# Kernel optimization log

Measured on AMD Instinct MI355X. Metric: run time of the kernel, lower is better.

## Reference

```python
import jax, jax.numpy as jnp
import numpy as np
from jax import lax

NUM_CLASSES = 20
NUM_ANCHORS = 5
COORDS = 4
NMS_TH = 0.45
PRE_TH = 0.005
FEAT_STRIDE = 32.0
BIASES = jnp.array([[1.08, 1.19], [3.42, 4.41], [6.63, 11.38],
                    [9.42, 5.11], [16.62, 10.52]], dtype=jnp.float32)  # [A,2]


def setup_inputs() -> dict:
    key = jax.random.key(0)
    B, H, W = 16, 26, 26
    C = (NUM_CLASSES + COORDS + 1) * NUM_ANCHORS  # 125
    x = jax.random.normal(key, (B, C, H, W), dtype=jnp.float32)
    im_info = jnp.array([480.0, 640.0], dtype=jnp.float32)  # (orig_h, orig_w)
    return {"x": x, "im_info": im_info}


def _pairwise_iou(b):
    # b: [N,4] center-format (cx, cy, w, h)
    x1 = b[:, 0] - b[:, 2] * 0.5
    y1 = b[:, 1] - b[:, 3] * 0.5
    x2 = b[:, 0] + b[:, 2] * 0.5
    y2 = b[:, 1] + b[:, 3] * 0.5
    area = (x2 - x1) * (y2 - y1)
    iw = jnp.maximum(jnp.minimum(x2[:, None], x2[None, :]) - jnp.maximum(x1[:, None], x1[None, :]), 0.0)
    ih = jnp.maximum(jnp.minimum(y2[:, None], y2[None, :]) - jnp.maximum(y1[:, None], y1[None, :]), 0.0)
    inter = iw * ih
    return inter / (area[:, None] + area[None, :] - inter + 1e-12)


def _nms_scores(boxes, scores):
    # greedy single-class NMS; returns scores with pre-threshold + suppressed boxes zeroed
    N = scores.shape[0]
    s = jnp.where(scores < PRE_TH, 0.0, scores)
    order = jnp.argsort(-s)
    ss = s[order]
    iou = lax.stop_gradient(_pairwise_iou(boxes[order]))  # [N,N]
    idx = jnp.arange(N)

    def body(i, keep):
        ki = keep[i] & (ss[i] > 0.0)
        sup = ki & (iou[i] > NMS_TH) & (idx > i)
        return keep & (~sup)

    keep_sorted = lax.fori_loop(0, N, body, jnp.ones((N,), dtype=bool))
    keep = jnp.zeros((N,), dtype=bool).at[order].set(keep_sorted)
    return jnp.where(keep, s, 0.0)


def _forward(x, im_info):
    B, C, H, W = x.shape
    A = NUM_ANCHORS
    fdt = x.dtype

    # --- Slice + activations (channel layout per SLICE_POINTS [10,20,25,125]) ---
    xy = jax.nn.sigmoid(x[:, :2 * A]).reshape(B, A, 2, H, W)
    wh = x[:, 2 * A:4 * A].reshape(B, A, 2, H, W)
    obj = jax.nn.sigmoid(x[:, 4 * A:5 * A])                    # [B,A,H,W]
    conf = x[:, 5 * A:].reshape(B, NUM_CLASSES, A, H, W)

    # --- class probability (plain softmax over class axis 1) + top predictions ---
    class_prob = jax.nn.softmax(conf, axis=1)                  # [B,C,A,H,W]
    top = class_prob * obj[:, None]                            # scale by objectness
    preds = jnp.concatenate([top, obj[:, None]], axis=1)       # [B,C+1,A,H,W]

    # --- YoloBBs: decode boxes on the grid, darknet correct_region_boxes ---
    col = jnp.arange(W, dtype=fdt)[None, None, None, :]
    row = jnp.arange(H, dtype=fdt)[None, None, :, None]
    bx = (col + xy[:, :, 0]) / W                               # [B,A,H,W]
    by = (row + xy[:, :, 1]) / H
    bw = BIASES[None, :, 0, None, None] * jnp.exp(wh[:, :, 0]) / W
    bh = BIASES[None, :, 1, None, None] * jnp.exp(wh[:, :, 1]) / H

    netw = W * FEAT_STRIDE
    neth = H * FEAT_STRIDE
    im_h, im_w = im_info[0], im_info[1]
    cond = (netw / im_w) < (neth / im_h)
    new_w = jnp.where(cond, netw, im_w * neth / im_h)
    new_h = jnp.where(cond, im_h * netw / im_w, neth)
    bx = (bx - (netw - new_w) * 0.5 / netw) / (new_w / netw)
    by = (by - (neth - new_h) * 0.5 / neth) / (new_h / neth)
    bw = bw * (netw / new_w)
    bh = bh * (neth / new_h)
    bboxs = jnp.stack([bx * im_w, by * im_h, bw * im_w, bh * im_h], axis=-1)
    N = A * H * W
    bboxs = bboxs.reshape(B, N, 4)                             # [B,N,4] (cx,cy,w,h) pixels

    # --- NMSFilter (classes=1, first_class=NUM_CLASSES -> objectness channel) ---
    preds_flat = preds.reshape(B, NUM_CLASSES + 1, N)
    obj_scores = preds_flat[:, NUM_CLASSES]                    # [B,N]
    new_obj = jax.vmap(_nms_scores)(bboxs, obj_scores)
    preds_flat = preds_flat.at[:, NUM_CLASSES].set(new_obj)

    # --- YoloEvalCompat: class axis moved last ---
    prob = jnp.transpose(preds_flat, (0, 2, 1))                # [B,N,C+1]
    return prob, bboxs


def reference(x, im_info):
    return _forward(x, im_info)
```

## Files before the change

kernel.cpp:

```cpp
#include <hip/hip_runtime.h>
#include <stdint.h>

#pragma clang fp contract(off)

#define NCLS   20
#define NA     5
#define NB     16
#define Hg     26
#define Wg     26
#define HWc    (Hg*Wg)
#define NBOX   (NA*HWc)
#define NPAD   4096
#define NWRD   (NPAD/64)
#define NROW   3392
#define SWRD   53
#define RGRP   27
#define PROBC  (NCLS+1)
#define PRE_TH 0.005f
#define NMS_TH 0.45f
#define ECHUNK 1024
#define ETOT   88192
#define SEGB(c) (32*(c)*((c)-1))

__constant__ float c_bias[10] = {1.08f,1.19f,3.42f,4.41f,6.63f,11.38f,9.42f,5.11f,16.62f,10.52f};

__device__ __forceinline__ unsigned long long rl64(unsigned long long v, int k) {
  unsigned int lo = (unsigned int)__builtin_amdgcn_readlane((int)(unsigned int)v, k);
  unsigned int hi = (unsigned int)__builtin_amdgcn_readlane((int)(unsigned int)(v >> 32), k);
  return ((unsigned long long)hi << 32) | lo;
}

__global__ __launch_bounds__(256) void k_decode(const float* __restrict__ x,
                                                const float* __restrict__ im_info,
                                                float* __restrict__ out,
                                                float* __restrict__ scores) {
  int t = blockIdx.x * 256 + threadIdx.x;
  if (t >= NB * NBOX) return;
  int b  = t / NBOX;
  int n  = t - b * NBOX;
  int a  = n / HWc;
  int hw = n - a * HWc;
  int h  = hw / Wg;
  int w  = hw - h * Wg;

  const float* xb = x + (size_t)b * 125 * HWc;
  float tx = xb[(2*a  ) * HWc + hw];
  float ty = xb[(2*a+1) * HWc + hw];
  float tw = xb[(10+2*a) * HWc + hw];
  float th = xb[(11+2*a) * HWc + hw];
  float to = xb[(20+a  ) * HWc + hw];

  float sx  = 1.0f / (1.0f + expf(-tx));
  float sy  = 1.0f / (1.0f + expf(-ty));
  float obj = 1.0f / (1.0f + expf(-to));

  float cf[NCLS];
  float mx = -3.402823e38f;
#pragma unroll
  for (int c = 0; c < NCLS; ++c) {
    cf[c] = xb[(25 + c*NA + a) * HWc + hw];
    mx = fmaxf(mx, cf[c]);
  }
  float sum = 0.f;
#pragma unroll
  for (int c = 0; c < NCLS; ++c) { cf[c] = expf(cf[c] - mx); sum += cf[c]; }

  float* op = out + ((size_t)b * NBOX + n) * PROBC;
#pragma unroll
  for (int c = 0; c < NCLS; ++c) op[c] = cf[c] / sum * obj;
  op[NCLS] = 0.f;

  float Wf = (float)Wg, Hf = (float)Hg;
  float bx = ((float)w + sx) / Wf;
  float by = ((float)h + sy) / Hf;
  float bw = c_bias[2*a]   * expf(tw) / Wf;
  float bh = c_bias[2*a+1] * expf(th) / Hf;
  float netw = Wf * 32.0f;
  float neth = Hf * 32.0f;
  float imh = im_info[0], imw = im_info[1];
  bool cond   = (netw / imw) < (neth / imh);
  float new_w = cond ? netw : (imw * neth / imh);
  float new_h = cond ? (imh * netw / imw) : neth;
  bx = (bx - (netw - new_w) * 0.5f / netw) / (new_w / netw);
  by = (by - (neth - new_h) * 0.5f / neth) / (new_h / neth);
  bw = bw * (netw / new_w);
  bh = bh * (neth / new_h);
  float X  = bx * imw, Y = by * imh, Wd = bw * imw, Hd = bh * imh;

  float* ob = out + (size_t)NB * NBOX * PROBC + ((size_t)b * NBOX + n) * 4;
  ob[0] = X; ob[1] = Y; ob[2] = Wd; ob[3] = Hd;

  scores[t] = (obj < PRE_TH) ? 0.f : obj;
}

__global__ __launch_bounds__(1024) void k_sort(const float* __restrict__ scores,
                                               const float* __restrict__ out,
                                               float* __restrict__ sScore,
                                               int* __restrict__ sIdx,
                                               float4* __restrict__ sBox,
                                               unsigned long long* __restrict__ posm,
                                               int* __restrict__ cnt) {
  int b    = blockIdx.x;
  int tid  = threadIdx.x;
  int lane = tid & 63;
  int wv   = tid >> 6;
  __shared__ unsigned long long key[NPAD];

  if (tid < SWRD) cnt[b * SWRD + tid] = 0;

  for (int i = tid; i < NPAD; i += 1024) {
    unsigned long long k = 0ULL;
    if (i < NBOX) {
      float s = scores[b * NBOX + i];
      unsigned int bits = __float_as_uint(s);
      k = ((unsigned long long)bits << 32) | (unsigned long long)(0xFFFFFFFFu - (unsigned)i);
    }
    key[i] = k;
  }
  __syncthreads();

  for (int k = 2; k <= 256; k <<= 1) {
    for (int j = k >> 1; j > 0; j >>= 1) {
#pragma unroll
      for (int qq = 0; qq < 2; ++qq) {
        int q  = lane + (qq << 6);
        int li = ((q & ~(j - 1)) << 1) | (q & (j - 1));
        int i  = (wv << 8) + li;
        int ix = i | j;
        bool desc = ((i & k) == 0);
        unsigned long long a = key[i], c = key[ix];
        bool sw = desc ? (a < c) : (a > c);
        if (sw) { key[i] = c; key[ix] = a; }
      }
      asm volatile("" ::: "memory");
    }
  }
  __syncthreads();

  for (int k = 512; k <= NPAD; k <<= 1) {
    for (int j = k >> 1; j >= 256; j >>= 1) {
#pragma unroll
      for (int qq = 0; qq < 2; ++qq) {
        int q  = tid + (qq << 10);
        int i  = ((q & ~(j - 1)) << 1) | (q & (j - 1));
        int ix = i | j;
        bool desc = ((i & k) == 0);
        unsigned long long a = key[i], c = key[ix];
        bool sw = desc ? (a < c) : (a > c);
        if (sw) { key[i] = c; key[ix] = a; }
      }
      __syncthreads();
    }
    {
      bool desc = (((wv << 8) & k) == 0);
      for (int j = 128; j > 0; j >>= 1) {
#pragma unroll
        for (int qq = 0; qq < 2; ++qq) {
          int q  = lane + (qq << 6);
          int li = ((q & ~(j - 1)) << 1) | (q & (j - 1));
          int i  = (wv << 8) + li;
          int ix = i | j;
          unsigned long long a = key[i], c = key[ix];
          bool sw = desc ? (a < c) : (a > c);
          if (sw) { key[i] = c; key[ix] = a; }
        }
        asm volatile("" ::: "memory");
      }
      __syncthreads();
    }
  }

  const float4* outBox = (const float4*)(out + (size_t)NB * NBOX * PROBC);
  for (int i = tid; i < NPAD; i += 1024) {
    unsigned long long k = key[i];
    float s = __uint_as_float((unsigned)(k >> 32));
    bool pos = (k >> 32) != 0ULL;
    unsigned long long bal = __ballot(pos);
    if ((tid & 63) == 0) posm[b * NWRD + (i >> 6)] = bal;
    sScore[b * NPAD + i] = s;
    int oi = (int)(0xFFFFFFFFu - (unsigned)(k & 0xFFFFFFFFu));
    sIdx[b * NPAD + i] = oi;
    float4 bx = make_float4(0.f, 0.f, 0.f, 0.f);
    if (oi >= 0 && oi < NBOX) bx = outBox[(size_t)b * NBOX + oi];
    sBox[b * NPAD + i] = bx;
  }
}

__global__ __launch_bounds__(64) void k_supmat(const float4* __restrict__ sBox,
                                               unsigned long long* __restrict__ diag,
                                               ulonglong2* __restrict__ entries,
                                               int* __restrict__ cnt) {
  int colg = blockIdx.x;
  int rg   = blockIdx.y;
  if (colg < 2 * rg) return;
  int b = blockIdx.z;
  int l = threadIdx.x;

  __shared__ float4 corn[64];
  __shared__ float  carTH[64];

  float4 cb = sBox[(size_t)b * NPAD + colg * 64 + l];
  float c1 = cb.x - cb.z * 0.5f;
  float d1 = cb.y - cb.w * 0.5f;
  float c2 = cb.x + cb.z * 0.5f;
  float d2 = cb.y + cb.w * 0.5f;
  corn[l]  = make_float4(c1, d1, c2, d2);
  carTH[l] = NMS_TH * ((c2 - c1) * (d2 - d1));
  __syncthreads();

  int row0 = rg * 128 + l;
  int row1 = row0 + 64;
  float4 r0 = sBox[(size_t)b * NPAD + row0];
  float4 r1 = sBox[(size_t)b * NPAD + row1];
  float a0x1 = r0.x - r0.z * 0.5f, a0y1 = r0.y - r0.w * 0.5f;
  float a0x2 = r0.x + r0.z * 0.5f, a0y2 = r0.y + r0.w * 0.5f;
  float a1x1 = r1.x - r1.z * 0.5f, a1y1 = r1.y - r1.w * 0.5f;
  float a1x2 = r1.x + r1.z * 0.5f, a1y2 = r1.y + r1.w * 0.5f;
  float rc0 = NMS_TH * ((a0x2 - a0x1) * (a0y2 - a0y1) + 1e-12f);
  float rc1 = NMS_TH * ((a1x2 - a1x1) * (a1y2 - a1y1) + 1e-12f);
  const float OPT = 1.0f + NMS_TH;

  unsigned long long bits0 = 0ULL, bits1 = 0ULL;
#pragma unroll 4
  for (int t2 = 0; t2 < 64; ++t2) {
    float4 cc = corn[t2];
    float ct  = carTH[t2];
    float iw0 = fmaxf(fminf(a0x2, cc.z) - fmaxf(a0x1, cc.x), 0.0f);
    float ih0 = fmaxf(fminf(a0y2, cc.w) - fmaxf(a0y1, cc.y), 0.0f);
    float iw1 = fmaxf(fminf(a1x2, cc.z) - fmaxf(a1x1, cc.x), 0.0f);
    float ih1 = fmaxf(fminf(a1y2, cc.w) - fmaxf(a1y1, cc.y), 0.0f);
    bool s0 = (iw0 * ih0) * OPT > rc0 + ct;
    bool s1 = (iw1 * ih1) * OPT > rc1 + ct;
    bits0 |= s0 ? (1ULL << t2) : 0ULL;
    bits1 |= s1 ? (1ULL << t2) : 0ULL;
  }

  unsigned long long selfmask = (l < 63) ? ((~0ULL) << (l + 1)) : 0ULL;
  if (colg == 2 * rg) {
    diag[((size_t)b * SWRD + colg) * 64 + l] = bits0 & selfmask;
  } else if (colg == 2 * rg + 1) {
    if (bits0) {
      int p = atomicAdd(&cnt[b * SWRD + colg], 1);
      entries[(size_t)b * ETOT + SEGB(colg) + p] =
          ulonglong2{(unsigned long long)row0, bits0};
    }
    diag[((size_t)b * SWRD + colg) * 64 + l] = bits1 & selfmask;
  } else {
    if (bits0) {
      int p = atomicAdd(&cnt[b * SWRD + colg], 1);
      entries[(size_t)b * ETOT + SEGB(colg) + p] =
          ulonglong2{(unsigned long long)row0, bits0};
    }
    if (bits1) {
      int p = atomicAdd(&cnt[b * SWRD + colg], 1);
      entries[(size_t)b * ETOT + SEGB(colg) + p] =
          ulonglong2{(unsigned long long)row1, bits1};
    }
  }
}

__global__ __launch_bounds__(512) void k_scan(const unsigned long long* __restrict__ diag,
                                              const ulonglong2* __restrict__ entries,
                                              const int* __restrict__ cnt,
                                              const unsigned long long* __restrict__ posm,
                                              const float* __restrict__ sScore,
                                              const int* __restrict__ sIdx,
                                              float* __restrict__ out) {
  int b    = blockIdx.x;
  int tid  = threadIdx.x;
  int lane = tid & 63;
  int wid  = tid >> 6;
  __shared__ unsigned long long diagS[SWRD * 64];
  __shared__ unsigned long long bitsE[2][ECHUNK];
  __shared__ unsigned short     rowE[2][ECHUNK];
  __shared__ unsigned long long remv[SWRD];
  __shared__ int cntS[SWRD];

  const ulonglong2* segB = entries + (size_t)b * ETOT;

  if (tid < SWRD) {
    remv[tid] = ~posm[b * NWRD + tid];
    cntS[tid] = cnt[b * SWRD + tid];
  }
  for (int i = tid; i < SWRD * 64; i += 512)
    diagS[i] = diag[(size_t)b * SWRD * 64 + i];
  __syncthreads();

  for (int c = 0; c < SWRD; ++c) {
    if (wid > 0) {
      if (c + 1 < SWRD) {
        int nn = cntS[c + 1];
        if (nn > ECHUNK) nn = ECHUNK;
        const ulonglong2* sp = segB + SEGB(c + 1);
        int buf = (c + 1) & 1;
        for (int g = tid - 64; g < nn; g += 448) {
          ulonglong2 e = sp[g];
          bitsE[buf][g] = e.y;
          rowE[buf][g]  = (unsigned short)e.x;
        }
      }
    } else {
      int nc = cntS[c];
      int nl = nc > ECHUNK ? ECHUNK : nc;
      int buf = c & 1;
      unsigned long long acc = 0ULL;
      for (int g = lane; g < nl; g += 64) {
        int row = rowE[buf][g];
        if (!((remv[row >> 6] >> (row & 63)) & 1ULL)) acc |= bitsE[buf][g];
      }
      for (int g = ECHUNK + lane; g < nc; g += 64) {
        ulonglong2 e = segB[SEGB(c) + g];
        int row = (int)e.x;
        if (!((remv[row >> 6] >> (row & 63)) & 1ULL)) acc |= e.y;
      }
#pragma unroll
      for (int off = 32; off >= 1; off >>= 1) acc |= __shfl_xor(acc, off);

      unsigned long long cur = remv[c] | acc;
      unsigned long long dg  = diagS[(c << 6) + lane];

      unsigned long long m = __ballot(dg != 0ULL) & ~cur;
      while (m) {
        int k = __ffsll((long long)m) - 1;
        cur |= rl64(dg, k);
        m &= m - 1;
        m &= ~cur;
      }
      if (lane == 0) remv[c] = cur;
    }
    __syncthreads();
  }

  for (int p = tid; p < NBOX; p += 512) {
    if (!((remv[p >> 6] >> (p & 63)) & 1ULL)) {
      int oi  = sIdx[b * NPAD + p];
      float s = sScore[b * NPAD + p];
      out[((size_t)b * NBOX + oi) * PROBC + NCLS] = s;
    }
  }
}

extern "C" void kernel_launch(void* const* d_in, const int* in_sizes, int n_in,
                              void* d_out, int out_size, void* d_ws, size_t ws_size,
                              hipStream_t stream) {
  const float* x  = (const float*)d_in[0];
  const float* im = (const float*)d_in[1];
  float* out = (float*)d_out;

  float* scores = (float*)d_ws;
  float* sScore = scores + (size_t)NB * NBOX;
  int*   sIdx   = (int*)(sScore + (size_t)NB * NPAD);
  float4* sBox  = (float4*)(sIdx + (size_t)NB * NPAD);
  unsigned long long* posm = (unsigned long long*)(sBox + (size_t)NB * NPAD);
  unsigned long long* diag = posm + (size_t)NB * NWRD;
  int* cnt = (int*)(diag + (size_t)NB * SWRD * 64);
  ulonglong2* entries = (ulonglong2*)((char*)cnt + (((size_t)NB * SWRD * 4 + 15) & ~(size_t)15));

  hipLaunchKernelGGL(k_decode, dim3((NB * NBOX + 255) / 256), dim3(256), 0, stream,
                     x, im, out, scores);
  hipLaunchKernelGGL(k_sort, dim3(NB), dim3(1024), 0, stream,
                     scores, out, sScore, sIdx, sBox, posm, cnt);
  hipLaunchKernelGGL(k_supmat, dim3(SWRD, RGRP, NB), dim3(64), 0, stream,
                     sBox, diag, entries, cnt);
  hipLaunchKernelGGL(k_scan, dim3(NB), dim3(512), 0, stream,
                     diag, entries, cnt, posm, sScore, sIdx, out);
}
```

Before: 196.2 us.

## Collapse NMS scan to a single wavefront without block barriers

The scan kernel goes from 512 threads, where seven producer waves double-buffer entries into shared memory, to a single 64-lane wave that reads entries straight from global memory. This removes the per-chunk __syncthreads barrier from the serial loop over 53 column words. Bounds checks on rows, counts and output indices are added in both the suppression-matrix and scan kernels. The trade-off is that global load latency now sits on the serial critical path with no prefetch, and diag staging uses fewer threads.

```diff
diff --git a/kernel.cpp b/kernel.cpp
--- a/kernel.cpp
+++ b/kernel.cpp
@@ -18,7 +18,6 @@
 #define PROBC  (NCLS+1)
 #define PRE_TH 0.005f
 #define NMS_TH 0.45f
-#define ECHUNK 1024
 #define ETOT   88192
 #define SEGB(c) (32*(c)*((c)-1))
 
@@ -239,103 +238,97 @@
   if (colg == 2 * rg) {
     diag[((size_t)b * SWRD + colg) * 64 + l] = bits0 & selfmask;
   } else if (colg == 2 * rg + 1) {
-    if (bits0) {
+    if (bits0 && row0 < NROW) {
       int p = atomicAdd(&cnt[b * SWRD + colg], 1);
-      entries[(size_t)b * ETOT + SEGB(colg) + p] =
-          ulonglong2{(unsigned long long)row0, bits0};
+      if (p < 64 * colg)
+        entries[(size_t)b * ETOT + SEGB(colg) + p] =
+            ulonglong2{(unsigned long long)row0, bits0};
     }
     diag[((size_t)b * SWRD + colg) * 64 + l] = bits1 & selfmask;
   } else {
-    if (bits0) {
+    if (bits0 && row0 < NROW) {
       int p = atomicAdd(&cnt[b * SWRD + colg], 1);
-      entries[(size_t)b * ETOT + SEGB(colg) + p] =
-          ulonglong2{(unsigned long long)row0, bits0};
-    }
-    if (bits1) {
+      if (p < 64 * colg)
+        entries[(size_t)b * ETOT + SEGB(colg) + p] =
+            ulonglong2{(unsigned long long)row0, bits0};
+    }
+    if (bits1 && row1 < NROW) {
       int p = atomicAdd(&cnt[b * SWRD + colg], 1);
-      entries[(size_t)b * ETOT + SEGB(colg) + p] =
-          ulonglong2{(unsigned long long)row1, bits1};
-    }
-  }
-}
-
-__global__ __launch_bounds__(512) void k_scan(const unsigned long long* __restrict__ diag,
-                                              const ulonglong2* __restrict__ entries,
-                                              const int* __restrict__ cnt,
-                                              const unsigned long long* __restrict__ posm,
-                                              const float* __restrict__ sScore,
-                                              const int* __restrict__ sIdx,
-                                              float* __restrict__ out) {
+      if (p < 64 * colg)
+        entries[(size_t)b * ETOT + SEGB(colg) + p] =
+            ulonglong2{(unsigned long long)row1, bits1};
+    }
+  }
+}
+
+__global__ __launch_bounds__(64) void k_scan(const unsigned long long* __restrict__ diag,
+                                             const ulonglong2* __restrict__ entries,
+                                             const int* __restrict__ cnt,
+                                             const unsigned long long* __restrict__ posm,
+                                             const float* __restrict__ sScore,
+                                             const int* __restrict__ sIdx,
+                                             float* __restrict__ out) {
   int b    = blockIdx.x;
-  int tid  = threadIdx.x;
-  int lane = tid & 63;
-  int wid  = tid >> 6;
+  int lane = threadIdx.x;
+
   __shared__ unsigned long long diagS[SWRD * 64];
-  __shared__ unsigned long long bitsE[2][ECHUNK];
-  __shared__ unsigned short     rowE[2][ECHUNK];
   __shared__ unsigned long long remv[SWRD];
-  __shared__ int cntS[SWRD];
+  __shared__ int offs[SWRD + 1];
 
   const ulonglong2* segB = entries + (size_t)b * ETOT;
 
-  if (tid < SWRD) {
-    remv[tid] = ~posm[b * NWRD + tid];
-    cntS[tid] = cnt[b * SWRD + tid];
-  }
-  for (int i = tid; i < SWRD * 64; i += 512)
+  if (lane < SWRD) remv[lane] = ~posm[b * NWRD + lane];
+  for (int i = lane; i < SWRD * 64; i += 64)
     diagS[i] = diag[(size_t)b * SWRD * 64 + i];
+
+  {
+    int v = (lane < SWRD) ? cnt[b * SWRD + lane] : 0;
+    if (v < 0) v = 0;
+    int s = v;
+#pragma unroll
+    for (int d = 1; d < 64; d <<= 1) {
+      int o = __shfl_up(s, d);
+      if (lane >= d) s += o;
+    }
+    if (lane < SWRD) offs[lane + 1] = s;
+    if (lane == 0)  offs[0] = 0;
+  }
   __syncthreads();
 
   for (int c = 0; c < SWRD; ++c) {
-    if (wid > 0) {
-      if (c + 1 < SWRD) {
-        int nn = cntS[c + 1];
-        if (nn > ECHUNK) nn = ECHUNK;
-        const ulonglong2* sp = segB + SEGB(c + 1);
-        int buf = (c + 1) & 1;
-        for (int g = tid - 64; g < nn; g += 448) {
-          ulonglong2 e = sp[g];
-          bitsE[buf][g] = e.y;
-          rowE[buf][g]  = (unsigned short)e.x;
-        }
-      }
-    } else {
-      int nc = cntS[c];
-      int nl = nc > ECHUNK ? ECHUNK : nc;
-      int buf = c & 1;
-      unsigned long long acc = 0ULL;
-      for (int g = lane; g < nl; g += 64) {
-        int row = rowE[buf][g];
-        if (!((remv[row >> 6] >> (row & 63)) & 1ULL)) acc |= bitsE[buf][g];
-      }
-      for (int g = ECHUNK + lane; g < nc; g += 64) {
-        ulonglong2 e = segB[SEGB(c) + g];
-        int row = (int)e.x;
-        if (!((remv[row >> 6] >> (row & 63)) & 1ULL)) acc |= e.y;
-      }
-#pragma unroll
-      for (int off = 32; off >= 1; off >>= 1) acc |= __shfl_xor(acc, off);
-
-      unsigned long long cur = remv[c] | acc;
-      unsigned long long dg  = diagS[(c << 6) + lane];
-
-      unsigned long long m = __ballot(dg != 0ULL) & ~cur;
-      while (m) {
-        int k = __ffsll((long long)m) - 1;
-        cur |= rl64(dg, k);
-        m &= m - 1;
-        m &= ~cur;
-      }
-      if (lane == 0) remv[c] = cur;
-    }
-    __syncthreads();
-  }
-
-  for (int p = tid; p < NBOX; p += 512) {
+    int ne = offs[c + 1] - offs[c];
+    int cap = c << 6;
+    if (ne > cap) ne = cap;
+    unsigned long long acc = 0ULL;
+    for (int g = lane; g < ne; g += 64) {
+      ulonglong2 e = segB[SEGB(c) + g];
+      unsigned int row = (unsigned int)e.x;
+      if (row < (unsigned)NROW &&
+          !((remv[row >> 6] >> (row & 63)) & 1ULL)) acc |= e.y;
+    }
+#pragma unroll
+    for (int off = 32; off >= 1; off >>= 1) acc |= __shfl_xor(acc, off);
+
+    unsigned long long cur = remv[c] | acc;
+    unsigned long long dg  = diagS[(c << 6) + lane];
+
+    unsigned long long m = __ballot(dg != 0ULL) & ~cur;
+    while (m) {
+      int k = __ffsll((long long)m) - 1;
+      cur |= rl64(dg, k);
+      m &= m - 1;
+      m &= ~cur;
+    }
+    if (lane == 0) remv[c] = cur;
+    asm volatile("" ::: "memory");
+  }
+
+  for (int p = lane; p < NBOX; p += 64) {
     if (!((remv[p >> 6] >> (p & 63)) & 1ULL)) {
       int oi  = sIdx[b * NPAD + p];
       float s = sScore[b * NPAD + p];
-      out[((size_t)b * NBOX + oi) * PROBC + NCLS] = s;
+      if (oi >= 0 && oi < NBOX)
+        out[((size_t)b * NBOX + oi) * PROBC + NCLS] = s;
     }
   }
 }
@@ -362,6 +355,6 @@
                      scores, out, sScore, sIdx, sBox, posm, cnt);
   hipLaunchKernelGGL(k_supmat, dim3(SWRD, RGRP, NB), dim3(64), 0, stream,
                      sBox, diag, entries, cnt);
-  hipLaunchKernelGGL(k_scan, dim3(NB), dim3(512), 0, stream,
+  hipLaunchKernelGGL(k_scan, dim3(NB), dim3(64), 0, stream,
                      diag, entries, cnt, posm, sScore, sIdx, out);
 }
```

New measurement: 266.0 us. 1.36x slower.
